# Performance work log

Hardware: AMD Instinct MI355X
Metric: run time of the kernel (lower is better)

The kernel has to match this reference:

```python
import jax, jax.numpy as jnp
import numpy as np


def setup_inputs() -> dict:
    key = jax.random.key(0)
    k1, k2 = jax.random.split(key)
    B, C, H, W = 16, 4, 768, 768
    img = jax.random.normal(k1, (B, C, H, W), dtype=jnp.float32)
    # dense displacement field (voxel units), 2 channels for (y, x) with 'ij' indexing
    trf = jax.random.normal(k2, (B, 2, H, W), dtype=jnp.float32)
    return {"img": img, "trf": trf}


def _warp_linear(vol, disp):
    # vol:  [B, H, W, C]   disp: [B, H, W, 2] (ij displacements)
    B, H, W, C = vol.shape
    dt = vol.dtype
    gy, gx = jnp.meshgrid(jnp.arange(H, dtype=dt), jnp.arange(W, dtype=dt), indexing='ij')
    loc = jnp.stack([gy, gx], axis=-1)[None] + disp          # absolute sample locations [B,H,W,2]
    max_loc = jnp.array([H - 1, W - 1], dtype=dt)
    clipped = jnp.clip(loc, 0.0, max_loc)
    loc0 = jnp.clip(jnp.floor(loc), 0.0, max_loc)
    loc1 = jnp.clip(loc0 + 1.0, 0.0, max_loc)
    d1 = loc1 - clipped                                       # weight of the floor corner (neurite convention)
    d0 = 1.0 - d1                                             # weight of the ceil corner
    i0 = loc0.astype(jnp.int32)
    i1 = loc1.astype(jnp.int32)
    vol_flat = vol.reshape(B, H * W, C)

    def gather(iy, ix):
        flat = (iy * W + ix).reshape(B, H * W)
        return jnp.take_along_axis(vol_flat, flat[..., None], axis=1).reshape(B, H, W, C)

    corners = [
        (i0[..., 0], d1[..., 0], i0[..., 1], d1[..., 1]),
        (i0[..., 0], d1[..., 0], i1[..., 1], d0[..., 1]),
        (i1[..., 0], d0[..., 0], i0[..., 1], d1[..., 1]),
        (i1[..., 0], d0[..., 0], i1[..., 1], d0[..., 1]),
    ]
    out = jnp.zeros_like(vol)
    for iy, wy, ix, wx in corners:
        out = out + (wy * wx)[..., None] * gather(iy, ix)
    return out


def reference(img, trf):
    # faithful to SpatialTransformer.forward with a dense 2D warp, 'ij' indexing,
    # linear interpolation, fill_value=None (edge clamping), single_transform=False
    vol = jnp.transpose(img, (0, 2, 3, 1))   # [B,H,W,C]
    disp = jnp.transpose(trf, (0, 2, 3, 1))  # [B,H,W,2]
    out = _warp_linear(vol, disp)
    return jnp.transpose(out, (0, 3, 1, 2))  # back to [B,C,H,W]
```

## Files before the change

kernel.cpp:

```cpp
#include <hip/hip_runtime.h>


typedef float fvec4 __attribute__((ext_vector_type(4)));

#define BB 16
#define CC 4
#define HH 768
#define WW 768
#define HWSZ (HH * WW)

#define TW 64
#define TH 32
#define HALO 8
#define TLW (TW + 2 * HALO)
#define TLH (TH + 2 * HALO)
#define LSTR 84
#define SLICE (TLH * LSTR)
#define NCHK (TLH * (TLW / 4))
#define TCHK (CC * NCHK)
#define NXT (WW / TW)
#define NYT (HH / TH)
#define TILES_PER_B (NXT * NYT)
#define NTILES (TILES_PER_B * BB)
#define NXCD 8
#define NTHR 512

__global__ __launch_bounds__(NTHR) void st_warp_lds4(
    const float* __restrict__ img,
    const float* __restrict__ trf,
    float* __restrict__ out)
{
    __shared__ float lds[CC * SLICE];

    int l = blockIdx.x;
    int xcd = l & (NXCD - 1);
    int t = xcd * (NTILES / NXCD) + (l >> 3);
    int b = t / TILES_PER_B;
    int rem = t - b * TILES_PER_B;
    int wt = rem / NYT;
    int ht = rem - wt * NYT;
    int h0 = ht * TH, w0 = wt * TW;
    int oy = h0 - HALO, ox = w0 - HALO;

    const float* ib = img + (size_t)b * CC * HWSZ;
    const float* tb = trf + (size_t)b * 2 * HWSZ;
    float* ob = out + (size_t)b * CC * HWSZ;

    int tid = threadIdx.x;
    int rrow = tid >> 4;
    int xg = tid & 15;
    int h = h0 + rrow;
    int x0 = w0 + xg * 4;

    int ptr0 = h * WW + x0;
    fvec4 dy4 = __builtin_nontemporal_load(reinterpret_cast<const fvec4*>(tb + ptr0));
    fvec4 dx4 = __builtin_nontemporal_load(reinterpret_cast<const fvec4*>(tb + HWSZ + ptr0));

#pragma unroll
    for (int i = 0; i < (TCHK + NTHR - 1) / NTHR; ++i) {
        int s = tid + i * NTHR;
        if (s < TCHK) {
            int c = s / NCHK;
            int r = s - c * NCHK;
            int ly = r / (TLW / 4);
            int g = r - ly * (TLW / 4);
            int lx0 = g * 4;
            int gy = min(max(oy + ly, 0), HH - 1);
            int gxr = ox + lx0;
            int gx0 = min(max(gxr, 0), WW - 4);
            fvec4 v = *reinterpret_cast<const fvec4*>(ib + (size_t)c * HWSZ + gy * WW + gx0);
            if (gxr != gx0) {
                fvec4 u;
#pragma unroll
                for (int j = 0; j < 4; ++j) {
                    int d = min(max(gxr + j, 0), WW - 1) - gx0;
                    u[j] = v[d];
                }
                v = u;
            }
            *reinterpret_cast<fvec4*>(&lds[c * SLICE + ly * LSTR + lx0]) = v;
        }
    }
    __syncthreads();

    const float maxy = (float)(HH - 1);
    const float maxx = (float)(WW - 1);

    float o0[4], o1[4], o2[4], o3[4];

#pragma unroll
    for (int j = 0; j < 4; ++j) {
        float y = (float)h + dy4[j];
        float x = (float)(x0 + j) + dx4[j];

        float cy = fminf(fmaxf(y, 0.0f), maxy);
        float cx = fminf(fmaxf(x, 0.0f), maxx);

        float f0y = fminf(fmaxf(floorf(y), 0.0f), maxy);
        float f0x = fminf(fmaxf(floorf(x), 0.0f), maxx);
        float f1y = fminf(f0y + 1.0f, maxy);
        float f1x = fminf(f0x + 1.0f, maxx);

        float wy0 = f1y - cy;
        float wx0 = f1x - cx;
        float wy1 = 1.0f - wy0;
        float wx1 = 1.0f - wx0;

        int i0y = (int)f0y;
        int i0x = (int)f0x;
        int i1y = (int)f1y;
        int i1x = (int)f1x;

        float w00 = wy0 * wx0;
        float w01 = wy0 * wx1;
        float w10 = wy1 * wx0;
        float w11 = wy1 * wx1;

        if (i0y >= oy && i1y <= oy + TLH - 1 && i0x >= ox && i1x <= ox + TLW - 1) {
            int a00 = (i0y - oy) * LSTR + (i0x - ox);
            int ddx = i1x - i0x;
            int ddy = (i1y - i0y) * LSTR;
            int a01 = a00 + ddx;
            int a10 = a00 + ddy;
            int a11 = a10 + ddx;
            o0[j] = w00 * lds[a00] + w01 * lds[a01] + w10 * lds[a10] + w11 * lds[a11];
            o1[j] = w00 * lds[SLICE + a00] + w01 * lds[SLICE + a01]
                  + w10 * lds[SLICE + a10] + w11 * lds[SLICE + a11];
            o2[j] = w00 * lds[2 * SLICE + a00] + w01 * lds[2 * SLICE + a01]
                  + w10 * lds[2 * SLICE + a10] + w11 * lds[2 * SLICE + a11];
            o3[j] = w00 * lds[3 * SLICE + a00] + w01 * lds[3 * SLICE + a01]
                  + w10 * lds[3 * SLICE + a10] + w11 * lds[3 * SLICE + a11];
        } else {
            int g00 = i0y * WW + i0x;
            int g01 = i0y * WW + i1x;
            int g10 = i1y * WW + i0x;
            int g11 = i1y * WW + i1x;
            o0[j] = w00 * ib[g00] + w01 * ib[g01] + w10 * ib[g10] + w11 * ib[g11];
            o1[j] = w00 * ib[HWSZ + g00] + w01 * ib[HWSZ + g01]
                  + w10 * ib[HWSZ + g10] + w11 * ib[HWSZ + g11];
            o2[j] = w00 * ib[2 * HWSZ + g00] + w01 * ib[2 * HWSZ + g01]
                  + w10 * ib[2 * HWSZ + g10] + w11 * ib[2 * HWSZ + g11];
            o3[j] = w00 * ib[3 * HWSZ + g00] + w01 * ib[3 * HWSZ + g01]
                  + w10 * ib[3 * HWSZ + g10] + w11 * ib[3 * HWSZ + g11];
        }
    }

    fvec4 s0 = { o0[0], o0[1], o0[2], o0[3] };
    fvec4 s1 = { o1[0], o1[1], o1[2], o1[3] };
    fvec4 s2 = { o2[0], o2[1], o2[2], o2[3] };
    fvec4 s3 = { o3[0], o3[1], o3[2], o3[3] };
    __builtin_nontemporal_store(s0, reinterpret_cast<fvec4*>(ob + ptr0));
    __builtin_nontemporal_store(s1, reinterpret_cast<fvec4*>(ob + HWSZ + ptr0));
    __builtin_nontemporal_store(s2, reinterpret_cast<fvec4*>(ob + 2 * HWSZ + ptr0));
    __builtin_nontemporal_store(s3, reinterpret_cast<fvec4*>(ob + 3 * HWSZ + ptr0));
}

extern "C" void kernel_launch(void* const* d_in, const int* in_sizes, int n_in,
                              void* d_out, int out_size, void* d_ws, size_t ws_size,
                              hipStream_t stream) {
    const float* img = (const float*)d_in[0];
    const float* trf = (const float*)d_in[1];
    float* out = (float*)d_out;

    st_warp_lds4<<<NTILES, NTHR, 0, stream>>>(img, trf, out);
}
```

Measured before the change: 318.6 us.

## Store LDS tile channel-interleaved as float4 per pixel for vector gathers

Changes the shared-memory tile from four planar channel slices to one float4 per pixel holding all four channels. Pixels are spread over four planes by x mod 4 (with an odd plane stride) so a wave's 16-byte reads avoid bank conflicts. Each corner fetch becomes a single 128-bit LDS read instead of four scalar reads, cutting LDS instruction count. The load phase now fetches all four channels per chunk and transposes them in registers before storing, which adds some register pressure and index arithmetic.

```diff
diff --git a/kernel.cpp b/kernel.cpp
--- a/kernel.cpp
+++ b/kernel.cpp
@@ -14,10 +14,11 @@
 #define HALO 8
 #define TLW (TW + 2 * HALO)
 #define TLH (TH + 2 * HALO)
-#define LSTR 84
-#define SLICE (TLH * LSTR)
-#define NCHK (TLH * (TLW / 4))
-#define TCHK (CC * NCHK)
+#define TILE_PX (TLH * TLW)
+#define NCHK (TILE_PX / 4)
+#define CPR (TLW / 4)
+#define PLANE 961
+#define NSLOT (4 * PLANE)
 #define NXT (WW / TW)
 #define NYT (HH / TH)
 #define TILES_PER_B (NXT * NYT)
@@ -25,12 +26,16 @@
 #define NXCD 8
 #define NTHR 512
 
-__global__ __launch_bounds__(NTHR) void st_warp_lds4(
+__device__ __forceinline__ int slot_of(int s) {
+    return PLANE * (s & 3) + (s >> 2);
+}
+
+__global__ __launch_bounds__(NTHR) void st_warp_v4(
     const float* __restrict__ img,
     const float* __restrict__ trf,
     float* __restrict__ out)
 {
-    __shared__ float lds[CC * SLICE];
+    __shared__ fvec4 tile[NSLOT];
 
     int l = blockIdx.x;
     int xcd = l & (NXCD - 1);
@@ -51,42 +56,46 @@
     int xg = tid & 15;
     int h = h0 + rrow;
     int x0 = w0 + xg * 4;
+    int ptr0 = h * WW + x0;
 
-    int ptr0 = h * WW + x0;
     fvec4 dy4 = __builtin_nontemporal_load(reinterpret_cast<const fvec4*>(tb + ptr0));
     fvec4 dx4 = __builtin_nontemporal_load(reinterpret_cast<const fvec4*>(tb + HWSZ + ptr0));
 
 #pragma unroll
-    for (int i = 0; i < (TCHK + NTHR - 1) / NTHR; ++i) {
-        int s = tid + i * NTHR;
-        if (s < TCHK) {
-            int c = s / NCHK;
-            int r = s - c * NCHK;
-            int ly = r / (TLW / 4);
-            int g = r - ly * (TLW / 4);
-            int lx0 = g * 4;
-            int gy = min(max(oy + ly, 0), HH - 1);
-            int gxr = ox + lx0;
-            int gx0 = min(max(gxr, 0), WW - 4);
-            fvec4 v = *reinterpret_cast<const fvec4*>(ib + (size_t)c * HWSZ + gy * WW + gx0);
-            if (gxr != gx0) {
-                fvec4 u;
-#pragma unroll
-                for (int j = 0; j < 4; ++j) {
-                    int d = min(max(gxr + j, 0), WW - 1) - gx0;
-                    u[j] = v[d];
-                }
-                v = u;
-            }
-            *reinterpret_cast<fvec4*>(&lds[c * SLICE + ly * LSTR + lx0]) = v;
+    for (int pass = 0; pass < 2; ++pass) {
+        int q = tid + pass * NTHR;
+        if (pass == 1 && tid >= NCHK - NTHR) break;
+        int ly = q / CPR;
+        int lx0 = (q - ly * CPR) * 4;
+        int gy = min(max(oy + ly, 0), HH - 1);
+        int gxr = ox + lx0;
+        int gx0 = min(max(gxr, 0), WW - 4);
+        const float* base = ib + gy * WW + gx0;
+        fvec4 p0 = *reinterpret_cast<const fvec4*>(base);
+        fvec4 p1 = *reinterpret_cast<const fvec4*>(base + HWSZ);
+        fvec4 p2 = *reinterpret_cast<const fvec4*>(base + 2 * HWSZ);
+        fvec4 p3 = *reinterpret_cast<const fvec4*>(base + 3 * HWSZ);
+        if (gxr != gx0) {
+            int d0 = min(max(gxr + 0, 0), WW - 1) - gx0;
+            int d1 = min(max(gxr + 1, 0), WW - 1) - gx0;
+            int d2 = min(max(gxr + 2, 0), WW - 1) - gx0;
+            int d3 = min(max(gxr + 3, 0), WW - 1) - gx0;
+            p0 = fvec4{p0[d0], p0[d1], p0[d2], p0[d3]};
+            p1 = fvec4{p1[d0], p1[d1], p1[d2], p1[d3]};
+            p2 = fvec4{p2[d0], p2[d1], p2[d2], p2[d3]};
+            p3 = fvec4{p3[d0], p3[d1], p3[d2], p3[d3]};
         }
+        tile[0 * PLANE + q] = fvec4{p0[0], p1[0], p2[0], p3[0]};
+        tile[1 * PLANE + q] = fvec4{p0[1], p1[1], p2[1], p3[1]};
+        tile[2 * PLANE + q] = fvec4{p0[2], p1[2], p2[2], p3[2]};
+        tile[3 * PLANE + q] = fvec4{p0[3], p1[3], p2[3], p3[3]};
     }
     __syncthreads();
 
     const float maxy = (float)(HH - 1);
     const float maxx = (float)(WW - 1);
 
-    float o0[4], o1[4], o2[4], o3[4];
+    fvec4 res[4];
 
 #pragma unroll
     for (int j = 0; j < 4; ++j) {
@@ -117,38 +126,34 @@
         float w11 = wy1 * wx1;
 
         if (i0y >= oy && i1y <= oy + TLH - 1 && i0x >= ox && i1x <= ox + TLW - 1) {
-            int a00 = (i0y - oy) * LSTR + (i0x - ox);
+            int s00 = (i0y - oy) * TLW + (i0x - ox);
             int ddx = i1x - i0x;
-            int ddy = (i1y - i0y) * LSTR;
-            int a01 = a00 + ddx;
-            int a10 = a00 + ddy;
-            int a11 = a10 + ddx;
-            o0[j] = w00 * lds[a00] + w01 * lds[a01] + w10 * lds[a10] + w11 * lds[a11];
-            o1[j] = w00 * lds[SLICE + a00] + w01 * lds[SLICE + a01]
-                  + w10 * lds[SLICE + a10] + w11 * lds[SLICE + a11];
-            o2[j] = w00 * lds[2 * SLICE + a00] + w01 * lds[2 * SLICE + a01]
-                  + w10 * lds[2 * SLICE + a10] + w11 * lds[2 * SLICE + a11];
-            o3[j] = w00 * lds[3 * SLICE + a00] + w01 * lds[3 * SLICE + a01]
-                  + w10 * lds[3 * SLICE + a10] + w11 * lds[3 * SLICE + a11];
+            int s10 = s00 + (i1y - i0y) * TLW;
+            fvec4 c00 = tile[slot_of(s00)];
+            fvec4 c01 = tile[slot_of(s00 + ddx)];
+            fvec4 c10 = tile[slot_of(s10)];
+            fvec4 c11 = tile[slot_of(s10 + ddx)];
+            res[j] = w00 * c00 + w01 * c01 + w10 * c10 + w11 * c11;
         } else {
             int g00 = i0y * WW + i0x;
             int g01 = i0y * WW + i1x;
             int g10 = i1y * WW + i0x;
             int g11 = i1y * WW + i1x;
-            o0[j] = w00 * ib[g00] + w01 * ib[g01] + w10 * ib[g10] + w11 * ib[g11];
-            o1[j] = w00 * ib[HWSZ + g00] + w01 * ib[HWSZ + g01]
-                  + w10 * ib[HWSZ + g10] + w11 * ib[HWSZ + g11];
-            o2[j] = w00 * ib[2 * HWSZ + g00] + w01 * ib[2 * HWSZ + g01]
-                  + w10 * ib[2 * HWSZ + g10] + w11 * ib[2 * HWSZ + g11];
-            o3[j] = w00 * ib[3 * HWSZ + g00] + w01 * ib[3 * HWSZ + g01]
-                  + w10 * ib[3 * HWSZ + g10] + w11 * ib[3 * HWSZ + g11];
+            fvec4 v;
+#pragma unroll
+            for (int c = 0; c < CC; ++c) {
+                const float* ic = ib + c * HWSZ;
+                v[c] = w00 * ic[g00] + w01 * ic[g01]
+                     + w10 * ic[g10] + w11 * ic[g11];
+            }
+            res[j] = v;
         }
     }
 
-    fvec4 s0 = { o0[0], o0[1], o0[2], o0[3] };
-    fvec4 s1 = { o1[0], o1[1], o1[2], o1[3] };
-    fvec4 s2 = { o2[0], o2[1], o2[2], o2[3] };
-    fvec4 s3 = { o3[0], o3[1], o3[2], o3[3] };
+    fvec4 s0 = {res[0][0], res[1][0], res[2][0], res[3][0]};
+    fvec4 s1 = {res[0][1], res[1][1], res[2][1], res[3][1]};
+    fvec4 s2 = {res[0][2], res[1][2], res[2][2], res[3][2]};
+    fvec4 s3 = {res[0][3], res[1][3], res[2][3], res[3][3]};
     __builtin_nontemporal_store(s0, reinterpret_cast<fvec4*>(ob + ptr0));
     __builtin_nontemporal_store(s1, reinterpret_cast<fvec4*>(ob + HWSZ + ptr0));
     __builtin_nontemporal_store(s2, reinterpret_cast<fvec4*>(ob + 2 * HWSZ + ptr0));
@@ -162,5 +167,5 @@
     const float* trf = (const float*)d_in[1];
     float* out = (float*)d_out;
 
-    st_warp_lds4<<<NTILES, NTHR, 0, stream>>>(img, trf, out);
+    st_warp_v4<<<NTILES, NTHR, 0, stream>>>(img, trf, out);
 }
```

New measurement: 312.1 us. 2.0% less time.
